# Performance work log

Hardware: AMD Instinct MI355X
Metric: run time of the kernel (lower is better)

## Reference

```python
import jax, jax.numpy as jnp
import numpy as np

N, L, C, H, W, HEAD = 16, 256, 512, 32, 32, 16

def setup_inputs() -> dict:
    key = jax.random.key(0)
    ks = jax.random.split(key, 8)
    s = 0.02  # weight init scale
    return {
        "feature": jax.random.normal(ks[0], (N, C, H, W), jnp.float32),
        "token": jax.random.normal(ks[1], (N, L, C), jnp.float32),
        "wq": jax.random.normal(ks[2], (C, C), jnp.float32) * s,
        "bq": jax.random.normal(ks[3], (C,), jnp.float32) * s,
        "wk": jax.random.normal(ks[4], (C, C), jnp.float32) * s,
        "bk": jax.random.normal(ks[5], (C,), jnp.float32) * s,
        "wv": jax.random.normal(ks[6], (C, C), jnp.float32) * s,
        "bv": jax.random.normal(ks[7], (C,), jnp.float32) * s,
    }

def reference(feature, token, wq, bq, wk, bk, wv, bv):
    n, c, hgt, wid = feature.shape
    h = HEAD
    d = c // h
    l = token.shape[1]
    scale = jnp.asarray(np.sqrt(c / h), feature.dtype)
    tok = token.transpose(0, 2, 1)  # (N, C, L)
    # 1x1 conv projections == per-position GEMMs
    v = (jnp.einsum('ncl,dc->ndl', tok, wv) + bv[None, :, None]).reshape(n, h, d, l)
    k = (jnp.einsum('ncl,dc->ndl', tok, wk) + bk[None, :, None]).reshape(n, h, d, l)
    q = (jnp.einsum('nchw,dc->ndhw', feature, wq) + bq[None, :, None, None])
    q = q.reshape(n, h, d, hgt * wid).transpose(0, 1, 3, 2)  # (N, h, HW, d)
    scores = jnp.einsum('nhqd,nhdl->nhql', q, k) / scale  # (N, h, HW, L)
    coef = jax.nn.softmax(scores, axis=-1)
    proj = jnp.einsum('nhdl,nhql->nhdq', v, coef)  # (N, h, d, HW)
    return feature + proj.reshape(n, c, hgt, wid)
```

## Files before the change

### kernel.cpp

```cpp
#include <hip/hip_runtime.h>
#include <hip/hip_bf16.h>

#define N_ 16
#define L_ 256
#define C_ 512
#define HW_ 1024
#define HEADS_ 16
#define DH_ 32

typedef unsigned short u16;
typedef unsigned int u32;
typedef __attribute__((ext_vector_type(8))) short short8_t;
typedef __attribute__((ext_vector_type(4))) float f32x4;
typedef __attribute__((ext_vector_type(2))) unsigned int u32x2;

__device__ __forceinline__ u16 f2bs(float f) {
    union { float f; u32 i; } x; x.f = f;
    u32 r = x.i + 0x7fffu + ((x.i >> 16) & 1u);
    return (u16)(r >> 16);
}
__device__ __forceinline__ u32 cvt_pk_bf16(float lo, float hi) {
    u32 r;
    asm("v_cvt_pk_bf16_f32 %0, %1, %2" : "=v"(r) : "v"(lo), "v"(hi));
    return r;
}
__device__ __forceinline__ void cvt8(const float* __restrict__ src, void* dst) {
    float4 lo = *(const float4*)src;
    float4 hi = *(const float4*)(src + 4);
    union { u32 w[4]; short8_t v; } pk;
    pk.w[0] = cvt_pk_bf16(lo.x, lo.y);
    pk.w[1] = cvt_pk_bf16(lo.z, lo.w);
    pk.w[2] = cvt_pk_bf16(hi.x, hi.y);
    pk.w[3] = cvt_pk_bf16(hi.z, hi.w);
    *(short8_t*)dst = pk.v;
}
#define AS1(p) (const __attribute__((address_space(1))) void*)(p)
#define AS3(p) (__attribute__((address_space(3))) void*)(p)

__global__ __launch_bounds__(256) void prep_kernel(
    const float* __restrict__ token, const float* __restrict__ wq,
    const float* __restrict__ wk, const float* __restrict__ wv,
    u16* __restrict__ tokb, u16* __restrict__ wqb,
    u16* __restrict__ wkb, u16* __restrict__ wvb)
{
    const int idx = blockIdx.x * 256 + threadIdx.x;
    const float* s; u16* d; int off;
    if (idx < 524288)            { s = token; d = tokb; off = idx; }
    else if (idx < 524288+65536) { s = wq; d = wqb; off = idx - 524288; }
    else if (idx < 524288+131072){ s = wk; d = wkb; off = idx - 524288 - 65536; }
    else                         { s = wv; d = wvb; off = idx - 524288 - 131072; }
    float4 v = ((const float4*)s)[off];
    ushort4 w;
    w.x = f2bs(v.x); w.y = f2bs(v.y); w.z = f2bs(v.z); w.w = f2bs(v.w);
    ((ushort4*)d)[off] = w;
}

__global__ __launch_bounds__(256) void proj_kernel(
    const float* __restrict__ feature,
    const u16* __restrict__ tokb, const u16* __restrict__ wqb,
    const u16* __restrict__ wkb, const u16* __restrict__ wvb,
    const float* __restrict__ bq, const float* __restrict__ bk,
    const float* __restrict__ bv,
    u16* __restrict__ Qout, u16* __restrict__ Kout, u16* __restrict__ Vt)
{
    __shared__ __align__(16) unsigned char smem[36864];

    const int t = threadIdx.x;
    const int lane = t & 63, wid = t >> 6;
    const int i16 = lane & 15, g = lane >> 4;

    if (blockIdx.x < 256) {
        const int xcd = blockIdx.x & 7, j = blockIdx.x >> 3;
        const int m0 = (xcd * 4 + (j & 3)) * 128;
        const int n0 = (j >> 2) * 64;
        u16* Tok = (u16*)smem;
        u16* Bk  = (u16*)(smem + 16384);
        u16* Bv  = (u16*)(smem + 24576);
        u16 (*LTo)[72] = (u16(*)[72])smem;

        const int wm = wid >> 1, wn = wid & 1;
        const int r8 = t >> 3, gr = t & 7;

        f32x4 ak[4][2], av[4][2];
        #pragma unroll
        for (int mt = 0; mt < 4; ++mt)
            #pragma unroll
            for (int nt = 0; nt < 2; ++nt) {
                ak[mt][nt] = (f32x4){0.f, 0.f, 0.f, 0.f};
                av[mt][nt] = (f32x4){0.f, 0.f, 0.f, 0.f};
            }

        for (int c0 = 0; c0 < C_; c0 += 64) {
            __syncthreads();
            #pragma unroll
            for (int p = 0; p < 4; ++p) {
                const int row = p * 32 + r8;
                __builtin_amdgcn_global_load_lds(
                    AS1(tokb + (size_t)(m0 + row) * C_ + c0 + ((gr ^ (row & 7)) << 3)),
                    AS3(smem + (p * 32 + wid * 8) * 128), 16, 0, 0);
            }
            #pragma unroll
            for (int p = 0; p < 2; ++p) {
                const int row = p * 32 + r8;
                const int gs = (gr ^ (row & 7)) << 3;
                __builtin_amdgcn_global_load_lds(
                    AS1(wkb + (size_t)(n0 + row) * C_ + c0 + gs),
                    AS3(smem + 16384 + (p * 32 + wid * 8) * 128), 16, 0, 0);
                __builtin_amdgcn_global_load_lds(
                    AS1(wvb + (size_t)(n0 + row) * C_ + c0 + gs),
                    AS3(smem + 24576 + (p * 32 + wid * 8) * 128), 16, 0, 0);
            }
            __syncthreads();
            #pragma unroll
            for (int ks = 0; ks < 2; ++ks) {
                short8_t a[4], bbk[2], bbv[2];
                #pragma unroll
                for (int mt = 0; mt < 4; ++mt) {
                    const int m = wm * 64 + mt * 16 + i16;
                    a[mt] = *(const short8_t*)&Tok[m * 64 + ((((ks << 2) | g) ^ (m & 7)) << 3)];
                }
                #pragma unroll
                for (int nt = 0; nt < 2; ++nt) {
                    const int d = wn * 32 + nt * 16 + i16;
                    const int sw = d * 64 + ((((ks << 2) | g) ^ (d & 7)) << 3);
                    bbk[nt] = *(const short8_t*)&Bk[sw];
                    bbv[nt] = *(const short8_t*)&Bv[sw];
                }
                #pragma unroll
                for (int mt = 0; mt < 4; ++mt)
                    #pragma unroll
                    for (int nt = 0; nt < 2; ++nt) {
                        ak[mt][nt] = __builtin_amdgcn_mfma_f32_16x16x32_bf16(
                            a[mt], bbk[nt], ak[mt][nt], 0, 0, 0);
                        av[mt][nt] = __builtin_amdgcn_mfma_f32_16x16x32_bf16(
                            a[mt], bbv[nt], av[mt][nt], 0, 0, 0);
                    }
            }
        }
        const int nb = m0 >> 8, l0 = m0 & 255;
        const size_t vtbase = (size_t)nb * C_ * L_;
        #pragma unroll
        for (int nt = 0; nt < 2; ++nt) {
            const int d = n0 + wn * 32 + nt * 16 + i16;
            const float bb = bv[d];
            #pragma unroll
            for (int mt = 0; mt < 4; ++mt) {
                ushort4 w;
                w.x = f2bs(av[mt][nt][0] + bb);
                w.y = f2bs(av[mt][nt][1] + bb);
                w.z = f2bs(av[mt][nt][2] + bb);
                w.w = f2bs(av[mt][nt][3] + bb);
                const int l = l0 + wm * 64 + mt * 16 + g * 4;
                *(ushort4*)&Vt[vtbase + (size_t)d * L_ + l] = w;
            }
        }
        __syncthreads();
        #pragma unroll
        for (int nt = 0; nt < 2; ++nt) {
            const int col = wn * 32 + nt * 16 + i16;
            const float bb = bk[n0 + col];
            #pragma unroll
            for (int mt = 0; mt < 4; ++mt)
                #pragma unroll
                for (int r = 0; r < 4; ++r)
                    LTo[wm * 64 + mt * 16 + g * 4 + r][col] =
                        f2bs(ak[mt][nt][r] + bb);
        }
        __syncthreads();
        #pragma unroll
        for (int rep = 0; rep < 4; ++rep) {
            const int m = (t >> 3) + rep * 32;
            const int cs = (t & 7) * 8;
            *(short8_t*)&Kout[(size_t)(m0 + m) * C_ + n0 + cs] = *(short8_t*)&LTo[m][cs];
        }
    } else {
        const int qid = blockIdx.x - 256;
        const int xcd = qid & 7, j = qid >> 3;
        const int m0 = (xcd * 16 + (j & 15)) * 128;
        const int n0 = (j >> 4) * 128;
        const int n = m0 >> 10, pos0 = m0 & (HW_ - 1);
        u16* Wt = (u16*)smem;
        const int FB = 16384;

        const int wq_pos = wid >> 1, wq_d = wid & 1;
        const int r8 = t >> 3, gr = t & 7;

        f32x4 acc[4][4];
        #pragma unroll
        for (int dm = 0; dm < 4; ++dm)
            #pragma unroll
            for (int pf = 0; pf < 4; ++pf)
                acc[dm][pf] = (f32x4){0.f, 0.f, 0.f, 0.f};

        for (int c0 = 0; c0 < C_; c0 += 64) {
            __syncthreads();
            #pragma unroll
            for (int p = 0; p < 4; ++p) {
                const int row = p * 32 + r8;
                __builtin_amdgcn_global_load_lds(
                    AS1(wqb + (size_t)(n0 + row) * C_ + c0 + ((gr ^ (row & 7)) << 3)),
                    AS3(smem + (p * 32 + wid * 8) * 128), 16, 0, 0);
            }
            #pragma unroll
            for (int p = 0; p < 4; ++p) {
                const int row = p * 16 + (t >> 4);
                const int pos8 = (t & 15) * 8;
                float f8[8];
                *(float4*)&f8[0] = *(const float4*)&feature[
                    ((size_t)n * C_ + c0 + row) * HW_ + pos0 + pos8];
                *(float4*)&f8[4] = *(const float4*)&feature[
                    ((size_t)n * C_ + c0 + row) * HW_ + pos0 + pos8 + 4];
                const int cb = row >> 2, cr = row & 3;
                const int pb = pos8 >> 4, po = (pos8 & 15) * 2;
                cvt8(f8, smem + FB + (cb * 8 + pb) * 160 + cr * 32 + po);
            }
            __syncthreads();
            #pragma unroll
            for (int ks = 0; ks < 2; ++ks) {
                short8_t a[4], b[4];
                #pragma unroll
                for (int dm = 0; dm < 4; ++dm) {
                    const int m = wq_d * 64 + dm * 16 + i16;
                    a[dm] = *(const short8_t*)&Wt[m * 64 + ((((ks << 2) | g) ^ (m & 7)) << 3)];
                }
                #pragma unroll
                for (int pf = 0; pf < 4; ++pf) {
                    const int pb = wq_pos * 4 + pf;
                    const u32 vaddr = FB +
                        (u32)((ks * 8 + g * 2) * 8 + pb) * 160 + (u32)i16 * 2;
                    u32x2 lo, hi;
                    asm volatile("ds_read_b64_tr_b16 %0, %1"
                                 : "=v"(lo) : "v"(vaddr));
                    asm volatile("ds_read_b64_tr_b16 %0, %1 offset:1280"
                                 : "=v"(hi) : "v"(vaddr));
                    union { u32 w[4]; short8_t v; } pk;
                    pk.w[0] = lo[0]; pk.w[1] = lo[1];
                    pk.w[2] = hi[0]; pk.w[3] = hi[1];
                    b[pf] = pk.v;
                }
                asm volatile("s_waitcnt lgkmcnt(0)" ::: "memory");
                __builtin_amdgcn_sched_barrier(0);
                #pragma unroll
                for (int dm = 0; dm < 4; ++dm)
                    #pragma unroll
                    for (int pf = 0; pf < 4; ++pf)
                        acc[dm][pf] = __builtin_amdgcn_mfma_f32_16x16x32_bf16(
                            a[dm], b[pf], acc[dm][pf], 0, 0, 0);
            }
        }
        #pragma unroll
        for (int dm = 0; dm < 4; ++dm) {
            const int dbase = wq_d * 64 + dm * 16 + g * 4;
            float4 b4 = *(const float4*)&bq[n0 + dbase];
            const float bb[4] = {b4.x, b4.y, b4.z, b4.w};
            #pragma unroll
            for (int pf = 0; pf < 4; ++pf) {
                const int pos = wq_pos * 64 + pf * 16 + i16;
                ushort4 w;
                w.x = f2bs(acc[dm][pf][0] + bb[0]);
                w.y = f2bs(acc[dm][pf][1] + bb[1]);
                w.z = f2bs(acc[dm][pf][2] + bb[2]);
                w.w = f2bs(acc[dm][pf][3] + bb[3]);
                *(ushort4*)&Qout[(size_t)(m0 + pos) * C_ + n0 + dbase] = w;
            }
        }
    }
}

__global__ __launch_bounds__(256) void attn_kernel(
    const u16* __restrict__ Qws, const u16* __restrict__ Kws,
    const u16* __restrict__ Vws, const float* __restrict__ feature,
    float* __restrict__ out)
{
    __shared__ __align__(16) unsigned char smem[32768];

    const int t = threadIdx.x;
    const int wid = t >> 6, lane = t & 63;
    const int i16 = lane & 15, g = lane >> 4;
    const int pt = blockIdx.x, h = blockIdx.y, n = blockIdx.z;
    const int pos0 = pt * 64;
    const size_t qbase = ((size_t)n * HW_ + pos0) * C_ + h * DH_;
    const size_t kbase = ((size_t)n * L_) * C_ + h * DH_;
    const size_t vbase = (size_t)n * C_ * L_ + (size_t)h * DH_ * L_;

    const int q = wid * 16 + i16;

    short8_t bq = *(const short8_t*)&Qws[qbase + (size_t)q * C_ + g * 8];

    #pragma unroll
    for (int p = 0; p < 4; ++p) {
        const int kg = (lane & 3) ^ ((lane >> 3) & 3);
        const int kr = wid * 64 + p * 16 + (lane >> 2);
        const u16* ksrc = Kws + kbase + (size_t)kr * C_ + kg * 8;
        __builtin_amdgcn_global_load_lds(AS1(ksrc),
            AS3(smem + wid * 4096 + p * 1024), 16, 0, 0);
        const int vd = wid * 8 + p * 2 + (lane >> 5);
        const u16* vsrc = Vws + vbase + (size_t)vd * L_ + ((lane & 31) ^ (vd & 7)) * 8;
        __builtin_amdgcn_global_load_lds(AS1(vsrc),
            AS3(smem + 16384 + wid * 4096 + p * 1024), 16, 0, 0);
    }
    __syncthreads();

    const int kgr = g ^ ((i16 >> 1) & 3);
    f32x4 s[16];
    #pragma unroll
    for (int nf = 0; nf < 16; ++nf) {
        short8_t a = *(const short8_t*)(smem + (nf * 16 + i16) * 64 + kgr * 16);
        f32x4 z = {0.f, 0.f, 0.f, 0.f};
        s[nf] = __builtin_amdgcn_mfma_f32_16x16x32_bf16(a, bq, z, 0, 0, 0);
    }

    float mm[16], sm[16];
    #pragma unroll
    for (int nf = 0; nf < 16; ++nf)
        mm[nf] = fmaxf(fmaxf(s[nf][0], s[nf][1]), fmaxf(s[nf][2], s[nf][3]));
    #pragma unroll
    for (int st = 8; st >= 1; st >>= 1)
        #pragma unroll
        for (int i = 0; i < 8; ++i)
            if (i < st) mm[i] = fmaxf(mm[i], mm[i + st]);
    float m = mm[0];
    m = fmaxf(m, __shfl_xor(m, 16));
    m = fmaxf(m, __shfl_xor(m, 32));

    const float K2 = 0.25506288f;
    #pragma unroll
    for (int nf = 0; nf < 16; ++nf) {
        #pragma unroll
        for (int r = 0; r < 4; ++r) s[nf][r] = exp2f((s[nf][r] - m) * K2);
        sm[nf] = (s[nf][0] + s[nf][1]) + (s[nf][2] + s[nf][3]);
    }
    #pragma unroll
    for (int st = 8; st >= 1; st >>= 1)
        #pragma unroll
        for (int i = 0; i < 8; ++i)
            if (i < st) sm[i] += sm[i + st];
    float ssum = sm[0];
    ssum += __shfl_xor(ssum, 16);
    ssum += __shfl_xor(ssum, 32);
    const float pinv = 1.0f / ssum;

    __syncthreads();

    f32x4 o0 = {0.f, 0.f, 0.f, 0.f}, o1 = {0.f, 0.f, 0.f, 0.f};
    const int e7 = i16 & 7;

    #pragma unroll
    for (int hb = 0; hb < 2; ++hb) {
        #pragma unroll
        for (int nfp = 0; nfp < 8; ++nfp) {
            const int nf = hb * 8 + nfp;
            #pragma unroll
            for (int w = 0; w < 2; ++w) {
                u32 pw = cvt_pk_bf16(s[nf][2 * w] * pinv, s[nf][2 * w + 1] * pinv);
                const int gran = (nfp * 2 + (g >> 1)) ^ e7;
                *(u32*)(smem + q * 256 + gran * 16 + ((g & 1) * 2 + w) * 4) = pw;
            }
        }
        __syncthreads();
        #pragma unroll
        for (int ks = 0; ks < 4; ++ks) {
            short8_t pb = *(const short8_t*)(smem + q * 256 + (((ks * 4 + g) ^ e7) * 16));
            const int vg = (((hb * 4 + ks) * 4 + g) ^ e7) * 16;
            short8_t va0 = *(const short8_t*)(smem + 16384 + i16 * 512 + vg);
            short8_t va1 = *(const short8_t*)(smem + 16384 + (16 + i16) * 512 + vg);
            o0 = __builtin_amdgcn_mfma_f32_16x16x32_bf16(va0, pb, o0, 0, 0, 0);
            o1 = __builtin_amdgcn_mfma_f32_16x16x32_bf16(va1, pb, o1, 0, 0, 0);
        }
        if (hb == 0) __syncthreads();
    }

    const size_t obase = ((size_t)n * C_ + h * DH_) * HW_ + pos0 + q;
    #pragma unroll
    for (int r = 0; r < 4; ++r) {
        const size_t oa = obase + (size_t)(g * 4 + r) * HW_;
        out[oa] = feature[oa] + o0[r];
        const size_t ob = obase + (size_t)(16 + g * 4 + r) * HW_;
        out[ob] = feature[ob] + o1[r];
    }
}

extern "C" void kernel_launch(void* const* d_in, const int* in_sizes, int n_in,
                              void* d_out, int out_size, void* d_ws, size_t ws_size,
                              hipStream_t stream)
{
    const float* feature = (const float*)d_in[0];
    const float* token   = (const float*)d_in[1];
    const float* wq      = (const float*)d_in[2];
    const float* bq      = (const float*)d_in[3];
    const float* wk      = (const float*)d_in[4];
    const float* bk      = (const float*)d_in[5];
    const float* wv      = (const float*)d_in[6];
    const float* bv      = (const float*)d_in[7];
    float* out = (float*)d_out;

    u16* Qws = (u16*)d_ws;
    u16* Kws = Qws + (size_t)N_ * HW_ * C_;
    u16* Vws = Kws + (size_t)N_ * L_ * C_;

    char* ob = (char*)d_out;
    u16* tokb = (u16*)(ob + (16u << 20));
    u16* wqb  = (u16*)(ob + (20u << 20));
    u16* wkb  = (u16*)(ob + (20u << 20) + 524288);
    u16* wvb  = (u16*)(ob + (20u << 20) + 1048576);

    prep_kernel<<<dim3(2816), 256, 0, stream>>>(token, wq, wk, wv,
                                                tokb, wqb, wkb, wvb);
    proj_kernel<<<dim3(768), 256, 0, stream>>>(feature, tokb, wqb, wkb, wvb,
                                               bq, bk, bv, Qws, Kws, Vws);
    attn_kernel<<<dim3(16, 16, 16), 256, 0, stream>>>(Qws, Kws, Vws, feature, out);
}
```

Before: 76.32 us.

## Fuse Q projection into attention kernel with pipelined feature/Wq staging

Removes the separate Q projection and its bf16 Q workspace round trip: each attention block now computes its own 64-position by 32-dim Q tile from feature and Wq, double-buffering feature chunks and Wq slices in LDS and overlapping the K/V loads with the last chunk. The fp32 feature slice for the residual add is stashed in LDS during the projection so the epilogue no longer re-reads feature from global memory. The grid is remapped for XCD locality. In exchange, feature is read once per head pair instead of once overall, LDS use rises to about 70KB per block, which lowers occupancy, and the Q projection uses only small per-wave MFMA tiles.

```diff
diff --git a/kernel.cpp b/kernel.cpp
--- a/kernel.cpp
+++ b/kernel.cpp
@@ -55,251 +55,239 @@
     ((ushort4*)d)[off] = w;
 }
 
-__global__ __launch_bounds__(256) void proj_kernel(
-    const float* __restrict__ feature,
-    const u16* __restrict__ tokb, const u16* __restrict__ wqb,
-    const u16* __restrict__ wkb, const u16* __restrict__ wvb,
-    const float* __restrict__ bq, const float* __restrict__ bk,
-    const float* __restrict__ bv,
-    u16* __restrict__ Qout, u16* __restrict__ Kout, u16* __restrict__ Vt)
+__global__ __launch_bounds__(256) void proj_kv_kernel(
+    const u16* __restrict__ tokb, const u16* __restrict__ wkb,
+    const u16* __restrict__ wvb, const float* __restrict__ bk,
+    const float* __restrict__ bv, u16* __restrict__ Kout, u16* __restrict__ Vt)
 {
-    __shared__ __align__(16) unsigned char smem[36864];
-
+    __shared__ __align__(16) unsigned char smem[32768];
     const int t = threadIdx.x;
     const int lane = t & 63, wid = t >> 6;
     const int i16 = lane & 15, g = lane >> 4;
-
-    if (blockIdx.x < 256) {
-        const int xcd = blockIdx.x & 7, j = blockIdx.x >> 3;
-        const int m0 = (xcd * 4 + (j & 3)) * 128;
-        const int n0 = (j >> 2) * 64;
-        u16* Tok = (u16*)smem;
-        u16* Bk  = (u16*)(smem + 16384);
-        u16* Bv  = (u16*)(smem + 24576);
-        u16 (*LTo)[72] = (u16(*)[72])smem;
-
-        const int wm = wid >> 1, wn = wid & 1;
-        const int r8 = t >> 3, gr = t & 7;
-
-        f32x4 ak[4][2], av[4][2];
-        #pragma unroll
-        for (int mt = 0; mt < 4; ++mt)
+    const int xcd = blockIdx.x & 7, j = blockIdx.x >> 3;
+    const int m0 = (xcd * 4 + (j & 3)) * 128;
+    const int n0 = (j >> 2) * 64;
+    u16* Tok = (u16*)smem;
+    u16* Bk  = (u16*)(smem + 16384);
+    u16* Bv  = (u16*)(smem + 24576);
+    u16 (*LTo)[72] = (u16(*)[72])smem;
+
+    const int wm = wid >> 1, wn = wid & 1;
+    const int r8 = t >> 3, gr = t & 7;
+
+    f32x4 ak[4][2], av[4][2];
+    #pragma unroll
+    for (int mt = 0; mt < 4; ++mt)
+        #pragma unroll
+        for (int nt = 0; nt < 2; ++nt) {
+            ak[mt][nt] = (f32x4){0.f, 0.f, 0.f, 0.f};
+            av[mt][nt] = (f32x4){0.f, 0.f, 0.f, 0.f};
+        }
+
+    for (int c0 = 0; c0 < C_; c0 += 64) {
+        __syncthreads();
+        #pragma unroll
+        for (int p = 0; p < 4; ++p) {
+            const int row = p * 32 + r8;
+            __builtin_amdgcn_global_load_lds(
+                AS1(tokb + (size_t)(m0 + row) * C_ + c0 + ((gr ^ (row & 7)) << 3)),
+                AS3(smem + (p * 32 + wid * 8) * 128), 16, 0, 0);
+        }
+        #pragma unroll
+        for (int p = 0; p < 2; ++p) {
+            const int row = p * 32 + r8;
+            const int gs = (gr ^ (row & 7)) << 3;
+            __builtin_amdgcn_global_load_lds(
+                AS1(wkb + (size_t)(n0 + row) * C_ + c0 + gs),
+                AS3(smem + 16384 + (p * 32 + wid * 8) * 128), 16, 0, 0);
+            __builtin_amdgcn_global_load_lds(
+                AS1(wvb + (size_t)(n0 + row) * C_ + c0 + gs),
+                AS3(smem + 24576 + (p * 32 + wid * 8) * 128), 16, 0, 0);
+        }
+        __syncthreads();
+        #pragma unroll
+        for (int ks = 0; ks < 2; ++ks) {
+            short8_t a[4], bbk[2], bbv[2];
+            #pragma unroll
+            for (int mt = 0; mt < 4; ++mt) {
+                const int m = wm * 64 + mt * 16 + i16;
+                a[mt] = *(const short8_t*)&Tok[m * 64 + ((((ks << 2) | g) ^ (m & 7)) << 3)];
+            }
             #pragma unroll
             for (int nt = 0; nt < 2; ++nt) {
-                ak[mt][nt] = (f32x4){0.f, 0.f, 0.f, 0.f};
-                av[mt][nt] = (f32x4){0.f, 0.f, 0.f, 0.f};
+                const int d = wn * 32 + nt * 16 + i16;
+                const int sw = d * 64 + ((((ks << 2) | g) ^ (d & 7)) << 3);
+                bbk[nt] = *(const short8_t*)&Bk[sw];
+                bbv[nt] = *(const short8_t*)&Bv[sw];
             }
-
-        for (int c0 = 0; c0 < C_; c0 += 64) {
-            __syncthreads();
-            #pragma unroll
-            for (int p = 0; p < 4; ++p) {
-                const int row = p * 32 + r8;
-                __builtin_amdgcn_global_load_lds(
-                    AS1(tokb + (size_t)(m0 + row) * C_ + c0 + ((gr ^ (row & 7)) << 3)),
-                    AS3(smem + (p * 32 + wid * 8) * 128), 16, 0, 0);
-            }
-            #pragma unroll
-            for (int p = 0; p < 2; ++p) {
-                const int row = p * 32 + r8;
-                const int gs = (gr ^ (row & 7)) << 3;
-                __builtin_amdgcn_global_load_lds(
-                    AS1(wkb + (size_t)(n0 + row) * C_ + c0 + gs),
-                    AS3(smem + 16384 + (p * 32 + wid * 8) * 128), 16, 0, 0);
-                __builtin_amdgcn_global_load_lds(
-                    AS1(wvb + (size_t)(n0 + row) * C_ + c0 + gs),
-                    AS3(smem + 24576 + (p * 32 + wid * 8) * 128), 16, 0, 0);
-            }
-            __syncthreads();
-            #pragma unroll
-            for (int ks = 0; ks < 2; ++ks) {
-                short8_t a[4], bbk[2], bbv[2];
-                #pragma unroll
-                for (int mt = 0; mt < 4; ++mt) {
-                    const int m = wm * 64 + mt * 16 + i16;
-                    a[mt] = *(const short8_t*)&Tok[m * 64 + ((((ks << 2) | g) ^ (m & 7)) << 3)];
-                }
+            #pragma unroll
+            for (int mt = 0; mt < 4; ++mt)
                 #pragma unroll
                 for (int nt = 0; nt < 2; ++nt) {
-                    const int d = wn * 32 + nt * 16 + i16;
-                    const int sw = d * 64 + ((((ks << 2) | g) ^ (d & 7)) << 3);
-                    bbk[nt] = *(const short8_t*)&Bk[sw];
-                    bbv[nt] = *(const short8_t*)&Bv[sw];
+                    ak[mt][nt] = __builtin_amdgcn_mfma_f32_16x16x32_bf16(
+                        a[mt], bbk[nt], ak[mt][nt], 0, 0, 0);
+                    av[mt][nt] = __builtin_amdgcn_mfma_f32_16x16x32_bf16(
+                        a[mt], bbv[nt], av[mt][nt], 0, 0, 0);
                 }
-                #pragma unroll
-                for (int mt = 0; mt < 4; ++mt)
-                    #pragma unroll
-                    for (int nt = 0; nt < 2; ++nt) {
-                        ak[mt][nt] = __builtin_amdgcn_mfma_f32_16x16x32_bf16(
-                            a[mt], bbk[nt], ak[mt][nt], 0, 0, 0);
-                        av[mt][nt] = __builtin_amdgcn_mfma_f32_16x16x32_bf16(
-                            a[mt], bbv[nt], av[mt][nt], 0, 0, 0);
-                    }
-            }
-        }
-        const int nb = m0 >> 8, l0 = m0 & 255;
-        const size_t vtbase = (size_t)nb * C_ * L_;
-        #pragma unroll
-        for (int nt = 0; nt < 2; ++nt) {
-            const int d = n0 + wn * 32 + nt * 16 + i16;
-            const float bb = bv[d];
-            #pragma unroll
-            for (int mt = 0; mt < 4; ++mt) {
-                ushort4 w;
-                w.x = f2bs(av[mt][nt][0] + bb);
-                w.y = f2bs(av[mt][nt][1] + bb);
-                w.z = f2bs(av[mt][nt][2] + bb);
-                w.w = f2bs(av[mt][nt][3] + bb);
-                const int l = l0 + wm * 64 + mt * 16 + g * 4;
-                *(ushort4*)&Vt[vtbase + (size_t)d * L_ + l] = w;
-            }
-        }
-        __syncthreads();
-        #pragma unroll
-        for (int nt = 0; nt < 2; ++nt) {
-            const int col = wn * 32 + nt * 16 + i16;
-            const float bb = bk[n0 + col];
-            #pragma unroll
-            for (int mt = 0; mt < 4; ++mt)
-                #pragma unroll
-                for (int r = 0; r < 4; ++r)
-                    LTo[wm * 64 + mt * 16 + g * 4 + r][col] =
-                        f2bs(ak[mt][nt][r] + bb);
-        }
-        __syncthreads();
-        #pragma unroll
-        for (int rep = 0; rep < 4; ++rep) {
-            const int m = (t >> 3) + rep * 32;
-            const int cs = (t & 7) * 8;
-            *(short8_t*)&Kout[(size_t)(m0 + m) * C_ + n0 + cs] = *(short8_t*)&LTo[m][cs];
-        }
-    } else {
-        const int qid = blockIdx.x - 256;
-        const int xcd = qid & 7, j = qid >> 3;
-        const int m0 = (xcd * 16 + (j & 15)) * 128;
-        const int n0 = (j >> 4) * 128;
-        const int n = m0 >> 10, pos0 = m0 & (HW_ - 1);
-        u16* Wt = (u16*)smem;
-        const int FB = 16384;
-
-        const int wq_pos = wid >> 1, wq_d = wid & 1;
-        const int r8 = t >> 3, gr = t & 7;
-
-        f32x4 acc[4][4];
-        #pragma unroll
-        for (int dm = 0; dm < 4; ++dm)
-            #pragma unroll
-            for (int pf = 0; pf < 4; ++pf)
-                acc[dm][pf] = (f32x4){0.f, 0.f, 0.f, 0.f};
-
-        for (int c0 = 0; c0 < C_; c0 += 64) {
-            __syncthreads();
-            #pragma unroll
-            for (int p = 0; p < 4; ++p) {
-                const int row = p * 32 + r8;
-                __builtin_amdgcn_global_load_lds(
-                    AS1(wqb + (size_t)(n0 + row) * C_ + c0 + ((gr ^ (row & 7)) << 3)),
-                    AS3(smem + (p * 32 + wid * 8) * 128), 16, 0, 0);
-            }
-            #pragma unroll
-            for (int p = 0; p < 4; ++p) {
-                const int row = p * 16 + (t >> 4);
-                const int pos8 = (t & 15) * 8;
-                float f8[8];
-                *(float4*)&f8[0] = *(const float4*)&feature[
-                    ((size_t)n * C_ + c0 + row) * HW_ + pos0 + pos8];
-                *(float4*)&f8[4] = *(const float4*)&feature[
-                    ((size_t)n * C_ + c0 + row) * HW_ + pos0 + pos8 + 4];
-                const int cb = row >> 2, cr = row & 3;
-                const int pb = pos8 >> 4, po = (pos8 & 15) * 2;
-                cvt8(f8, smem + FB + (cb * 8 + pb) * 160 + cr * 32 + po);
-            }
-            __syncthreads();
-            #pragma unroll
-            for (int ks = 0; ks < 2; ++ks) {
-                short8_t a[4], b[4];
-                #pragma unroll
-                for (int dm = 0; dm < 4; ++dm) {
-                    const int m = wq_d * 64 + dm * 16 + i16;
-                    a[dm] = *(const short8_t*)&Wt[m * 64 + ((((ks << 2) | g) ^ (m & 7)) << 3)];
-                }
-                #pragma unroll
-                for (int pf = 0; pf < 4; ++pf) {
-                    const int pb = wq_pos * 4 + pf;
-                    const u32 vaddr = FB +
-                        (u32)((ks * 8 + g * 2) * 8 + pb) * 160 + (u32)i16 * 2;
-                    u32x2 lo, hi;
-                    asm volatile("ds_read_b64_tr_b16 %0, %1"
-                                 : "=v"(lo) : "v"(vaddr));
-                    asm volatile("ds_read_b64_tr_b16 %0, %1 offset:1280"
-                                 : "=v"(hi) : "v"(vaddr));
-                    union { u32 w[4]; short8_t v; } pk;
-                    pk.w[0] = lo[0]; pk.w[1] = lo[1];
-                    pk.w[2] = hi[0]; pk.w[3] = hi[1];
-                    b[pf] = pk.v;
-                }
-                asm volatile("s_waitcnt lgkmcnt(0)" ::: "memory");
-                __builtin_amdgcn_sched_barrier(0);
-                #pragma unroll
-                for (int dm = 0; dm < 4; ++dm)
-                    #pragma unroll
-                    for (int pf = 0; pf < 4; ++pf)
-                        acc[dm][pf] = __builtin_amdgcn_mfma_f32_16x16x32_bf16(
-                            a[dm], b[pf], acc[dm][pf], 0, 0, 0);
-            }
-        }
-        #pragma unroll
-        for (int dm = 0; dm < 4; ++dm) {
-            const int dbase = wq_d * 64 + dm * 16 + g * 4;
-            float4 b4 = *(const float4*)&bq[n0 + dbase];
-            const float bb[4] = {b4.x, b4.y, b4.z, b4.w};
-            #pragma unroll
-            for (int pf = 0; pf < 4; ++pf) {
-                const int pos = wq_pos * 64 + pf * 16 + i16;
-                ushort4 w;
-                w.x = f2bs(acc[dm][pf][0] + bb[0]);
-                w.y = f2bs(acc[dm][pf][1] + bb[1]);
-                w.z = f2bs(acc[dm][pf][2] + bb[2]);
-                w.w = f2bs(acc[dm][pf][3] + bb[3]);
-                *(ushort4*)&Qout[(size_t)(m0 + pos) * C_ + n0 + dbase] = w;
-            }
-        }
+        }
+    }
+    const int nb = m0 >> 8, l0 = m0 & 255;
+    const size_t vtbase = (size_t)nb * C_ * L_;
+    #pragma unroll
+    for (int nt = 0; nt < 2; ++nt) {
+        const int d = n0 + wn * 32 + nt * 16 + i16;
+        const float bb = bv[d];
+        #pragma unroll
+        for (int mt = 0; mt < 4; ++mt) {
+            ushort4 w;
+            w.x = f2bs(av[mt][nt][0] + bb);
+            w.y = f2bs(av[mt][nt][1] + bb);
+            w.z = f2bs(av[mt][nt][2] + bb);
+            w.w = f2bs(av[mt][nt][3] + bb);
+            const int l = l0 + wm * 64 + mt * 16 + g * 4;
+            *(ushort4*)&Vt[vtbase + (size_t)d * L_ + l] = w;
+        }
+    }
+    __syncthreads();
+    #pragma unroll
+    for (int nt = 0; nt < 2; ++nt) {
+        const int col = wn * 32 + nt * 16 + i16;
+        const float bb = bk[n0 + col];
+        #pragma unroll
+        for (int mt = 0; mt < 4; ++mt)
+            #pragma unroll
+            for (int r = 0; r < 4; ++r)
+                LTo[wm * 64 + mt * 16 + g * 4 + r][col] = f2bs(ak[mt][nt][r] + bb);
+    }
+    __syncthreads();
+    #pragma unroll
+    for (int rep = 0; rep < 4; ++rep) {
+        const int m = (t >> 3) + rep * 32;
+        const int cs = (t & 7) * 8;
+        *(short8_t*)&Kout[(size_t)(m0 + m) * C_ + n0 + cs] = *(short8_t*)&LTo[m][cs];
     }
 }
 
 __global__ __launch_bounds__(256) void attn_kernel(
-    const u16* __restrict__ Qws, const u16* __restrict__ Kws,
-    const u16* __restrict__ Vws, const float* __restrict__ feature,
-    float* __restrict__ out)
+    const float* __restrict__ feature, const u16* __restrict__ wqb,
+    const float* __restrict__ bqv, const u16* __restrict__ Kws,
+    const u16* __restrict__ Vws, float* __restrict__ out)
 {
-    __shared__ __align__(16) unsigned char smem[32768];
+    __shared__ __align__(16) unsigned char smem[70144];
+    const u32 FEAT0 = 32768, WQ0 = 53248, STASH = 61440;
 
     const int t = threadIdx.x;
     const int wid = t >> 6, lane = t & 63;
     const int i16 = lane & 15, g = lane >> 4;
-    const int pt = blockIdx.x, h = blockIdx.y, n = blockIdx.z;
+    const int xcd = blockIdx.x & 7, local = blockIdx.x >> 3;
+    const int h = local & 15;
+    const int tile = (local >> 4) * 8 + xcd;
+    const int n = tile >> 4, pt = tile & 15;
     const int pos0 = pt * 64;
-    const size_t qbase = ((size_t)n * HW_ + pos0) * C_ + h * DH_;
+
     const size_t kbase = ((size_t)n * L_) * C_ + h * DH_;
     const size_t vbase = (size_t)n * C_ * L_ + (size_t)h * DH_ * L_;
-
     const int q = wid * 16 + i16;
 
-    short8_t bq = *(const short8_t*)&Qws[qbase + (size_t)q * C_ + g * 8];
-
-    #pragma unroll
-    for (int p = 0; p < 4; ++p) {
-        const int kg = (lane & 3) ^ ((lane >> 3) & 3);
-        const int kr = wid * 64 + p * 16 + (lane >> 2);
-        const u16* ksrc = Kws + kbase + (size_t)kr * C_ + kg * 8;
-        __builtin_amdgcn_global_load_lds(AS1(ksrc),
-            AS3(smem + wid * 4096 + p * 1024), 16, 0, 0);
-        const int vd = wid * 8 + p * 2 + (lane >> 5);
-        const u16* vsrc = Vws + vbase + (size_t)vd * L_ + ((lane & 31) ^ (vd & 7)) * 8;
-        __builtin_amdgcn_global_load_lds(AS1(vsrc),
-            AS3(smem + 16384 + wid * 4096 + p * 1024), 16, 0, 0);
-    }
+    const int frow = t >> 2, fpb = t & 3;
+    const int wrow = t >> 3, wgr = t & 7;
+    const int hh = h >> 1;
+
+    float f[16];
+    f32x4 aq0 = {0.f,0.f,0.f,0.f}, aq1 = {0.f,0.f,0.f,0.f};
+
+    #define LOADFEAT(c) { \
+        const float* src = &feature[((size_t)n * C_ + (c) * 64 + frow) * HW_ + pos0 + fpb * 16]; \
+        *(float4*)&f[0]  = *(const float4*)&src[0];  \
+        *(float4*)&f[4]  = *(const float4*)&src[4];  \
+        *(float4*)&f[8]  = *(const float4*)&src[8];  \
+        *(float4*)&f[12] = *(const float4*)&src[12]; }
+    #define STAGEWQ(c, buf) { \
+        __builtin_amdgcn_global_load_lds( \
+            AS1(wqb + (size_t)(h * 32 + wrow) * C_ + (c) * 64 + ((wgr ^ (wrow & 7)) << 3)), \
+            AS3(smem + WQ0 + (buf) * 4096 + wid * 1024), 16, 0, 0); }
+    #define WRITEFEAT(buf, dostash) { \
+        u32 pw[8]; \
+        _Pragma("unroll") \
+        for (int k2 = 0; k2 < 8; ++k2) pw[k2] = cvt_pk_bf16(f[2*k2], f[2*k2+1]); \
+        unsigned char* dst = smem + FEAT0 + (buf) * 10240 + \
+            (u32)(((frow >> 2) * 4 + fpb) * 160 + (frow & 3) * 32); \
+        *(short8_t*)dst = *(short8_t*)&pw[0]; \
+        *(short8_t*)(dst + 16) = *(short8_t*)&pw[4]; \
+        if ((dostash) && (frow >> 5) == (h & 1)) { \
+            unsigned char* sd = smem + STASH + (u32)((frow & 31) * 272 + fpb * 64); \
+            *(float4*)sd = *(float4*)&f[0]; \
+            *(float4*)(sd + 16) = *(float4*)&f[4]; \
+            *(float4*)(sd + 32) = *(float4*)&f[8]; \
+            *(float4*)(sd + 48) = *(float4*)&f[12]; } }
+    #define COMPUTECHUNK(buf) { \
+        _Pragma("unroll") \
+        for (int ks = 0; ks < 2; ++ks) { \
+            short8_t a0 = *(const short8_t*)(smem + WQ0 + (buf) * 4096 + \
+                (u32)(i16 * 128 + ((((ks << 2) | g) ^ (i16 & 7)) << 4))); \
+            short8_t a1 = *(const short8_t*)(smem + WQ0 + (buf) * 4096 + \
+                (u32)((16 + i16) * 128 + ((((ks << 2) | g) ^ (i16 & 7)) << 4))); \
+            const u32 vaddr = FEAT0 + (buf) * 10240 + \
+                (u32)(((ks * 8 + g * 2) * 4 + wid) * 160) + (u32)i16 * 2; \
+            u32x2 lo, hi; \
+            asm volatile("ds_read_b64_tr_b16 %0, %1" : "=v"(lo) : "v"(vaddr)); \
+            asm volatile("ds_read_b64_tr_b16 %0, %1 offset:640" : "=v"(hi) : "v"(vaddr)); \
+            union { u32 w[4]; short8_t v; } pk; \
+            pk.w[0] = lo[0]; pk.w[1] = lo[1]; pk.w[2] = hi[0]; pk.w[3] = hi[1]; \
+            asm volatile("s_waitcnt lgkmcnt(0)" ::: "memory"); \
+            __builtin_amdgcn_sched_barrier(0); \
+            aq0 = __builtin_amdgcn_mfma_f32_16x16x32_bf16(a0, pk.v, aq0, 0, 0, 0); \
+            aq1 = __builtin_amdgcn_mfma_f32_16x16x32_bf16(a1, pk.v, aq1, 0, 0, 0); } }
+
+    LOADFEAT(0);
+    STAGEWQ(0, 0);
+    WRITEFEAT(0, hh == 0);
     __syncthreads();
+    for (int c = 0; c < 8; ++c) {
+        const int cur = c & 1;
+        if (c < 7) {
+            LOADFEAT(c + 1);
+            STAGEWQ(c + 1, cur ^ 1);
+        } else {
+            #pragma unroll
+            for (int p = 0; p < 4; ++p) {
+                const int kg = (lane & 3) ^ ((lane >> 3) & 3);
+                const int kr = wid * 64 + p * 16 + (lane >> 2);
+                __builtin_amdgcn_global_load_lds(
+                    AS1(Kws + kbase + (size_t)kr * C_ + kg * 8),
+                    AS3(smem + wid * 4096 + p * 1024), 16, 0, 0);
+                const int vd = wid * 8 + p * 2 + (lane >> 5);
+                __builtin_amdgcn_global_load_lds(
+                    AS1(Vws + vbase + (size_t)vd * L_ + ((lane & 31) ^ (vd & 7)) * 8),
+                    AS3(smem + 16384 + wid * 4096 + p * 1024), 16, 0, 0);
+            }
+        }
+        COMPUTECHUNK(cur);
+        if (c < 7) WRITEFEAT(cur ^ 1, (c + 1) == hh);
+        __syncthreads();
+    }
+
+    short8_t bq;
+    {
+        float4 b0 = *(const float4*)&bqv[h * 32 + g * 4];
+        float4 b1 = *(const float4*)&bqv[h * 32 + 16 + g * 4];
+        u32 A0 = cvt_pk_bf16(aq0[0] + b0.x, aq0[1] + b0.y);
+        u32 A1 = cvt_pk_bf16(aq0[2] + b0.z, aq0[3] + b0.w);
+        u32 B0 = cvt_pk_bf16(aq1[0] + b1.x, aq1[1] + b1.y);
+        u32 B1 = cvt_pk_bf16(aq1[2] + b1.z, aq1[3] + b1.w);
+        const int srcLo = ((g & 1) * 2) * 16 + i16;
+        const int srcHi = srcLo + 16;
+        u32 XA0 = (u32)__shfl((int)A0, srcLo), XA1 = (u32)__shfl((int)A1, srcLo);
+        u32 XA2 = (u32)__shfl((int)A0, srcHi), XA3 = (u32)__shfl((int)A1, srcHi);
+        u32 XB0 = (u32)__shfl((int)B0, srcLo), XB1 = (u32)__shfl((int)B1, srcLo);
+        u32 XB2 = (u32)__shfl((int)B0, srcHi), XB3 = (u32)__shfl((int)B1, srcHi);
+        union { u32 w[4]; short8_t v; } bp;
+        bp.w[0] = g < 2 ? XA0 : XB0;
+        bp.w[1] = g < 2 ? XA1 : XB1;
+        bp.w[2] = g < 2 ? XA2 : XB2;
+        bp.w[3] = g < 2 ? XA3 : XB3;
+        bq = bp.v;
+    }
 
     const int kgr = g ^ ((i16 >> 1) & 3);
     f32x4 s[16];
@@ -373,10 +361,11 @@
     const size_t obase = ((size_t)n * C_ + h * DH_) * HW_ + pos0 + q;
     #pragma unroll
     for (int r = 0; r < 4; ++r) {
-        const size_t oa = obase + (size_t)(g * 4 + r) * HW_;
-        out[oa] = feature[oa] + o0[r];
-        const size_t ob = obase + (size_t)(16 + g * 4 + r) * HW_;
-        out[ob] = feature[ob] + o1[r];
+        const int d0 = g * 4 + r;
+        const float st0 = *(const float*)(smem + STASH + (u32)(d0 * 272 + q * 4));
+        out[obase + (size_t)d0 * HW_] = st0 + o0[r];
+        const float st1 = *(const float*)(smem + STASH + (u32)((16 + d0) * 272 + q * 4));
+        out[obase + (size_t)(16 + d0) * HW_] = st1 + o1[r];
     }
 }
 
@@ -394,19 +383,18 @@
     const float* bv      = (const float*)d_in[7];
     float* out = (float*)d_out;
 
-    u16* Qws = (u16*)d_ws;
-    u16* Kws = Qws + (size_t)N_ * HW_ * C_;
+    u16* Kws = (u16*)d_ws;
     u16* Vws = Kws + (size_t)N_ * L_ * C_;
+    u16* wqb = Vws + (size_t)N_ * L_ * C_;
 
     char* ob = (char*)d_out;
     u16* tokb = (u16*)(ob + (16u << 20));
-    u16* wqb  = (u16*)(ob + (20u << 20));
-    u16* wkb  = (u16*)(ob + (20u << 20) + 524288);
-    u16* wvb  = (u16*)(ob + (20u << 20) + 1048576);
+    u16* wkb  = (u16*)(ob + (20u << 20));
+    u16* wvb  = (u16*)(ob + (20u << 20) + 524288);
 
     prep_kernel<<<dim3(2816), 256, 0, stream>>>(token, wq, wk, wv,
                                                 tokb, wqb, wkb, wvb);
-    proj_kernel<<<dim3(768), 256, 0, stream>>>(feature, tokb, wqb, wkb, wvb,
-                                               bq, bk, bv, Qws, Kws, Vws);
-    attn_kernel<<<dim3(16, 16, 16), 256, 0, stream>>>(Qws, Kws, Vws, feature, out);
-}
+    proj_kv_kernel<<<dim3(256), 256, 0, stream>>>(tokb, wkb, wvb, bk, bv,
+                                                  Kws, Vws);
+    attn_kernel<<<dim3(4096), 256, 0, stream>>>(feature, wqb, bq, Kws, Vws, out);
+}
```

Result: slower. 110.0 us (+44.2%).

## Double-buffer Q projection loads and halve its M-tile to raise block count

Applied to the files above, without the earlier changes.

The Q-projection path of proj_kernel now uses 64-position tiles instead of 128, so the grid grows from 768 to 1280 blocks. It also double-buffers both the Wq tile (async global-to-LDS) and the feature tile (prefetched into registers, converted to bf16 on the next iteration), so global loads overlap the MFMA work. Shared memory grows to 53 KB, which may lower occupancy. Each block reloads Wq twice as often because the tile is smaller.

```diff
diff --git a/kernel.cpp b/kernel.cpp
--- a/kernel.cpp
+++ b/kernel.cpp
@@ -23,16 +23,6 @@
     u32 r;
     asm("v_cvt_pk_bf16_f32 %0, %1, %2" : "=v"(r) : "v"(lo), "v"(hi));
     return r;
-}
-__device__ __forceinline__ void cvt8(const float* __restrict__ src, void* dst) {
-    float4 lo = *(const float4*)src;
-    float4 hi = *(const float4*)(src + 4);
-    union { u32 w[4]; short8_t v; } pk;
-    pk.w[0] = cvt_pk_bf16(lo.x, lo.y);
-    pk.w[1] = cvt_pk_bf16(lo.z, lo.w);
-    pk.w[2] = cvt_pk_bf16(hi.x, hi.y);
-    pk.w[3] = cvt_pk_bf16(hi.z, hi.w);
-    *(short8_t*)dst = pk.v;
 }
 #define AS1(p) (const __attribute__((address_space(1))) void*)(p)
 #define AS3(p) (__attribute__((address_space(3))) void*)(p)
@@ -63,7 +53,7 @@
     const float* __restrict__ bv,
     u16* __restrict__ Qout, u16* __restrict__ Kout, u16* __restrict__ Vt)
 {
-    __shared__ __align__(16) unsigned char smem[36864];
+    __shared__ __align__(16) unsigned char smem[53248];
 
     const int t = threadIdx.x;
     const int lane = t & 63, wid = t >> 6;
@@ -163,8 +153,7 @@
             for (int mt = 0; mt < 4; ++mt)
                 #pragma unroll
                 for (int r = 0; r < 4; ++r)
-                    LTo[wm * 64 + mt * 16 + g * 4 + r][col] =
-                        f2bs(ak[mt][nt][r] + bb);
+                    LTo[wm * 64 + mt * 16 + g * 4 + r][col] = f2bs(ak[mt][nt][r] + bb);
         }
         __syncthreads();
         #pragma unroll
@@ -175,78 +164,93 @@
         }
     } else {
         const int qid = blockIdx.x - 256;
-        const int xcd = qid & 7, j = qid >> 3;
-        const int m0 = (xcd * 16 + (j & 15)) * 128;
-        const int n0 = (j >> 4) * 128;
+        const int xcd = qid & 7, loc = qid >> 3;
+        const int mtile = xcd * 32 + (loc >> 2);
+        const int nt4 = loc & 3;
+        const int m0 = mtile * 64;
+        const int n0 = nt4 * 128;
         const int n = m0 >> 10, pos0 = m0 & (HW_ - 1);
-        u16* Wt = (u16*)smem;
-        const int FB = 16384;
-
-        const int wq_pos = wid >> 1, wq_d = wid & 1;
+        const u32 FEAT0 = 32768;
+
+        const int wq_d = wid & 1, wq_pos = wid >> 1;
         const int r8 = t >> 3, gr = t & 7;
-
-        f32x4 acc[4][4];
+        const int frow = t >> 2, fpb = t & 3;
+
+        f32x4 acc[4][2];
         #pragma unroll
         for (int dm = 0; dm < 4; ++dm)
             #pragma unroll
-            for (int pf = 0; pf < 4; ++pf)
+            for (int pf = 0; pf < 2; ++pf)
                 acc[dm][pf] = (f32x4){0.f, 0.f, 0.f, 0.f};
 
-        for (int c0 = 0; c0 < C_; c0 += 64) {
+        float f[16];
+
+        #define QF_LOADFEAT(c) { \
+            const float* src = &feature[((size_t)n * C_ + (c) * 64 + frow) * HW_ + pos0 + fpb * 16]; \
+            *(float4*)&f[0]  = *(const float4*)&src[0];  \
+            *(float4*)&f[4]  = *(const float4*)&src[4];  \
+            *(float4*)&f[8]  = *(const float4*)&src[8];  \
+            *(float4*)&f[12] = *(const float4*)&src[12]; }
+        #define QF_STAGEWQ(c, buf) { \
+            _Pragma("unroll") \
+            for (int p = 0; p < 4; ++p) { \
+                const int row = p * 32 + r8; \
+                __builtin_amdgcn_global_load_lds( \
+                    AS1(wqb + (size_t)(n0 + row) * C_ + (c) * 64 + ((gr ^ (row & 7)) << 3)), \
+                    AS3(smem + (buf) * 16384 + (p * 32 + wid * 8) * 128), 16, 0, 0); } }
+        #define QF_WRITEFEAT(buf) { \
+            u32 pw[8]; \
+            _Pragma("unroll") \
+            for (int k2 = 0; k2 < 8; ++k2) pw[k2] = cvt_pk_bf16(f[2*k2], f[2*k2+1]); \
+            unsigned char* dst = smem + FEAT0 + (buf) * 10240 + \
+                (u32)(((frow >> 2) * 4 + fpb) * 160 + (frow & 3) * 32); \
+            *(short8_t*)dst = *(short8_t*)&pw[0]; \
+            *(short8_t*)(dst + 16) = *(short8_t*)&pw[4]; }
+
+        QF_LOADFEAT(0);
+        QF_STAGEWQ(0, 0);
+
+        for (int c = 0; c < 8; ++c) {
+            const int cur = c & 1;
+            QF_WRITEFEAT(cur);
+            if (c < 7) QF_LOADFEAT(c + 1);
             __syncthreads();
-            #pragma unroll
-            for (int p = 0; p < 4; ++p) {
-                const int row = p * 32 + r8;
-                __builtin_amdgcn_global_load_lds(
-                    AS1(wqb + (size_t)(n0 + row) * C_ + c0 + ((gr ^ (row & 7)) << 3)),
-                    AS3(smem + (p * 32 + wid * 8) * 128), 16, 0, 0);
-            }
-            #pragma unroll
-            for (int p = 0; p < 4; ++p) {
-                const int row = p * 16 + (t >> 4);
-                const int pos8 = (t & 15) * 8;
-                float f8[8];
-                *(float4*)&f8[0] = *(const float4*)&feature[
-                    ((size_t)n * C_ + c0 + row) * HW_ + pos0 + pos8];
-                *(float4*)&f8[4] = *(const float4*)&feature[
-                    ((size_t)n * C_ + c0 + row) * HW_ + pos0 + pos8 + 4];
-                const int cb = row >> 2, cr = row & 3;
-                const int pb = pos8 >> 4, po = (pos8 & 15) * 2;
-                cvt8(f8, smem + FB + (cb * 8 + pb) * 160 + cr * 32 + po);
-            }
-            __syncthreads();
-            #pragma unroll
-            for (int ks = 0; ks < 2; ++ks) {
-                short8_t a[4], b[4];
+            if (c < 7) QF_STAGEWQ(c + 1, cur ^ 1);
+            short8_t a2[2][4], b2[2][2];
+            #pragma unroll
+            for (int ks = 0; ks < 2; ++ks)
                 #pragma unroll
                 for (int dm = 0; dm < 4; ++dm) {
                     const int m = wq_d * 64 + dm * 16 + i16;
-                    a[dm] = *(const short8_t*)&Wt[m * 64 + ((((ks << 2) | g) ^ (m & 7)) << 3)];
+                    a2[ks][dm] = *(const short8_t*)(smem + cur * 16384 +
+                        (u32)(m * 128 + ((((ks << 2) | g) ^ (m & 7)) << 4)));
                 }
-                #pragma unroll
-                for (int pf = 0; pf < 4; ++pf) {
-                    const int pb = wq_pos * 4 + pf;
-                    const u32 vaddr = FB +
-                        (u32)((ks * 8 + g * 2) * 8 + pb) * 160 + (u32)i16 * 2;
+            #pragma unroll
+            for (int ks = 0; ks < 2; ++ks)
+                #pragma unroll
+                for (int pf = 0; pf < 2; ++pf) {
+                    const int pb = wq_pos * 2 + pf;
+                    const u32 vaddr = FEAT0 + cur * 10240 +
+                        (u32)(((ks * 8 + g * 2) * 4 + pb) * 160) + (u32)i16 * 2;
                     u32x2 lo, hi;
-                    asm volatile("ds_read_b64_tr_b16 %0, %1"
-                                 : "=v"(lo) : "v"(vaddr));
-                    asm volatile("ds_read_b64_tr_b16 %0, %1 offset:1280"
-                                 : "=v"(hi) : "v"(vaddr));
+                    asm volatile("ds_read_b64_tr_b16 %0, %1" : "=v"(lo) : "v"(vaddr));
+                    asm volatile("ds_read_b64_tr_b16 %0, %1 offset:640" : "=v"(hi) : "v"(vaddr));
                     union { u32 w[4]; short8_t v; } pk;
                     pk.w[0] = lo[0]; pk.w[1] = lo[1];
                     pk.w[2] = hi[0]; pk.w[3] = hi[1];
-                    b[pf] = pk.v;
+                    b2[ks][pf] = pk.v;
                 }
-                asm volatile("s_waitcnt lgkmcnt(0)" ::: "memory");
-                __builtin_amdgcn_sched_barrier(0);
+            asm volatile("s_waitcnt lgkmcnt(0)" ::: "memory");
+            __builtin_amdgcn_sched_barrier(0);
+            #pragma unroll
+            for (int ks = 0; ks < 2; ++ks)
                 #pragma unroll
                 for (int dm = 0; dm < 4; ++dm)
                     #pragma unroll
-                    for (int pf = 0; pf < 4; ++pf)
+                    for (int pf = 0; pf < 2; ++pf)
                         acc[dm][pf] = __builtin_amdgcn_mfma_f32_16x16x32_bf16(
-                            a[dm], b[pf], acc[dm][pf], 0, 0, 0);
-            }
+                            a2[ks][dm], b2[ks][pf], acc[dm][pf], 0, 0, 0);
+            __syncthreads();
         }
         #pragma unroll
         for (int dm = 0; dm < 4; ++dm) {
@@ -254,8 +258,8 @@
             float4 b4 = *(const float4*)&bq[n0 + dbase];
             const float bb[4] = {b4.x, b4.y, b4.z, b4.w};
             #pragma unroll
-            for (int pf = 0; pf < 4; ++pf) {
-                const int pos = wq_pos * 64 + pf * 16 + i16;
+            for (int pf = 0; pf < 2; ++pf) {
+                const int pos = wq_pos * 32 + pf * 16 + i16;
                 ushort4 w;
                 w.x = f2bs(acc[dm][pf][0] + bb[0]);
                 w.y = f2bs(acc[dm][pf][1] + bb[1]);
@@ -400,13 +404,13 @@
 
     char* ob = (char*)d_out;
     u16* tokb = (u16*)(ob + (16u << 20));
-    u16* wqb  = (u16*)(ob + (20u << 20));
-    u16* wkb  = (u16*)(ob + (20u << 20) + 524288);
-    u16* wvb  = (u16*)(ob + (20u << 20) + 1048576);
+    u16* wkb  = (u16*)(ob + (20u << 20));
+    u16* wvb  = (u16*)(ob + (20u << 20) + 524288);
+    u16* wqb  = (u16*)(ob + (21u << 20));
 
     prep_kernel<<<dim3(2816), 256, 0, stream>>>(token, wq, wk, wv,
                                                 tokb, wqb, wkb, wvb);
-    proj_kernel<<<dim3(768), 256, 0, stream>>>(feature, tokb, wqb, wkb, wvb,
-                                               bq, bk, bv, Qws, Kws, Vws);
+    proj_kernel<<<dim3(1280), 256, 0, stream>>>(feature, tokb, wqb, wkb, wvb,
+                                                bq, bk, bv, Qws, Kws, Vws);
     attn_kernel<<<dim3(16, 16, 16), 256, 0, stream>>>(Qws, Kws, Vws, feature, out);
 }
```

Result: faster. 71.63 us (-6.1%).
